# Kernel optimization log

Measured on AMD Instinct MI355X. Metric: run time of the kernel, lower is better.

Reference implementation:

```python
import jax, jax.numpy as jnp
import numpy as np

NQ, NKV, D = 32, 8, 64
HID = 2048
EPS = 1e-5
THETA = 1000000.0


def _rmsnorm(x, w):
    var = jnp.mean(x * x, axis=-1, keepdims=True)
    return x * jax.lax.rsqrt(var + EPS) * w


def setup_inputs() -> dict:
    key = jax.random.key(0)
    k1, k2, k3 = jax.random.split(key, 3)
    T = 2048
    positions = jnp.arange(T, dtype=jnp.int64) if jax.config.jax_enable_x64 else jnp.arange(T, dtype=jnp.int32)
    hidden_states = jax.random.normal(k1, (T, HID), dtype=jnp.float32)
    w_qkv = jax.random.normal(k2, (HID, (NQ + 2 * NKV) * D), dtype=jnp.float32) / np.sqrt(HID)
    w_out = jax.random.normal(k3, (NQ * D, HID), dtype=jnp.float32) / np.sqrt(NQ * D)
    q_ln_w = jnp.ones((D,), dtype=jnp.float32)
    k_ln_w = jnp.ones((D,), dtype=jnp.float32)
    return {"positions": positions, "hidden_states": hidden_states, "w_qkv": w_qkv,
            "w_out": w_out, "q_ln_w": q_ln_w, "k_ln_w": k_ln_w}


def reference(positions, hidden_states, w_qkv, w_out, q_ln_w, k_ln_w):
    T = hidden_states.shape[0]
    qkv = hidden_states @ w_qkv  # [T, (NQ+2*NKV)*D]
    q = qkv[:, : NQ * D].reshape(T, NQ, D)
    k = qkv[:, NQ * D : (NQ + NKV) * D].reshape(T, NKV, D)
    v = qkv[:, (NQ + NKV) * D :].reshape(T, NKV, D)
    # per-head RMSNorm on q and k
    q = _rmsnorm(q, q_ln_w)
    k = _rmsnorm(k, k_ln_w)
    # neox-style RoPE (rotate halves)
    inv_freq = 1.0 / (THETA ** (jnp.arange(0, D, 2, dtype=jnp.float32) / D))
    ang = positions.astype(jnp.float32)[:, None] * inv_freq  # [T, D/2]
    cos = jnp.cos(ang)[:, None, :]
    sin = jnp.sin(ang)[:, None, :]
    def rope(x):
        x1, x2 = x[..., : D // 2], x[..., D // 2 :]
        return jnp.concatenate([x1 * cos - x2 * sin, x2 * cos + x1 * sin], axis=-1)
    q = rope(q)
    k = rope(k)
    # grouped-query causal attention (one sequence, positions define order)
    G = NQ // NKV
    qg = q.reshape(T, NKV, G, D)
    scores = jnp.einsum('tkgd,skd->kgts', qg, k) * (D ** -0.5)  # [NKV,G,T,T]
    causal = jnp.arange(T)[:, None] >= jnp.arange(T)[None, :]
    scores = jnp.where(causal[None, None], scores, -1e30)
    probs = jax.nn.softmax(scores, axis=-1)
    attn = jnp.einsum('kgts,skd->tkgd', probs, v).reshape(T, NQ * D)
    return attn @ w_out
```

## Files before the change

kernel.cpp:

```cpp
#include <hip/hip_runtime.h>

typedef __bf16 bhalf;
typedef __bf16 bhalf8 __attribute__((ext_vector_type(8)));
typedef __bf16 bhalf4 __attribute__((ext_vector_type(4)));
typedef float f32x4 __attribute__((ext_vector_type(4)));

typedef __attribute__((address_space(1))) const void* gas_p;
typedef __attribute__((address_space(3))) void* las_p;

#define T_SEQ 2048
#define HIDN  2048
#define NQH   32
#define NKVH  8
#define DH    64
#define NQKV  3072

__global__ __launch_bounds__(256) void prep_k(const float* __restrict__ hidden,
                                              const float* __restrict__ w_qkv,
                                              const float* __restrict__ w_out,
                                              const int* __restrict__ pos,
                                              bhalf* __restrict__ hid_bf,
                                              bhalf* __restrict__ wqkvT,
                                              bhalf* __restrict__ woutT,
                                              float* __restrict__ rope) {
  __shared__ float tile[32][33];
  int bid = blockIdx.x;
  if (bid < 4096) {
    int i = (bid * 256 + threadIdx.x) * 4;
    float4 v = *(const float4*)(hidden + i);
    bhalf4 o;
    o[0] = (bhalf)v.x; o[1] = (bhalf)v.y; o[2] = (bhalf)v.z; o[3] = (bhalf)v.w;
    *(bhalf4*)(hid_bf + i) = o;
    return;
  }
  if (bid >= 14336) {
    int gid = (bid - 14336) * 256 + threadIdx.x;
    int t = gid >> 4, j = gid & 15;
    float p = (float)pos[t];
    float f0 = exp2f((float)j * -0.6228615177913804f);
    float a0 = p * f0, a1 = p * f0 * 0.001f;
    float4 cs = {cosf(a0), sinf(a0), cosf(a1), sinf(a1)};
    *(float4*)(rope + (size_t)gid * 4) = cs;
    return;
  }
  const float* in;
  bhalf* out;
  int R, C, bx, by;
  if (bid < 10240) {
    int b2 = bid - 4096;
    in = w_qkv; out = wqkvT; R = HIDN; C = NQKV;
    bx = (b2 % 96) * 32; by = (b2 / 96) * 32;
  } else {
    int b2 = bid - 10240;
    in = w_out; out = woutT; R = HIDN; C = HIDN;
    bx = (b2 % 64) * 32; by = (b2 / 64) * 32;
  }
  int tx = threadIdx.x & 31, ty = threadIdx.x >> 5;
#pragma unroll
  for (int p = 0; p < 4; ++p)
    tile[ty + 8 * p][tx] = in[(size_t)(by + ty + 8 * p) * C + bx + tx];
  __syncthreads();
#pragma unroll
  for (int p = 0; p < 4; ++p)
    out[(size_t)(bx + ty + 8 * p) * R + by + tx] = (bhalf)tile[tx][ty + 8 * p];
}

#define MFMA_BF16 __builtin_amdgcn_mfma_f32_16x16x32_bf16

#define GEMM_KS(ks)                                                            \
  {                                                                            \
    const int co_ = (((ks) * 4 + q4) ^ swz_) * 8;                              \
    bhalf8 af0 = *(const bhalf8*)&As[(wm_ +  0 + m16) * 64 + co_];             \
    bhalf8 af1 = *(const bhalf8*)&As[(wm_ + 16 + m16) * 64 + co_];             \
    bhalf8 af2 = *(const bhalf8*)&As[(wm_ + 32 + m16) * 64 + co_];             \
    bhalf8 af3 = *(const bhalf8*)&As[(wm_ + 48 + m16) * 64 + co_];             \
    bhalf8 bf0 = *(const bhalf8*)&Bs[(wn_ +  0 + m16) * 64 + co_];             \
    bhalf8 bf1 = *(const bhalf8*)&Bs[(wn_ + 16 + m16) * 64 + co_];             \
    bhalf8 bf2 = *(const bhalf8*)&Bs[(wn_ + 32 + m16) * 64 + co_];             \
    bhalf8 bf3 = *(const bhalf8*)&Bs[(wn_ + 48 + m16) * 64 + co_];             \
    acc[0][0] = MFMA_BF16(af0, bf0, acc[0][0], 0, 0, 0);                       \
    acc[0][1] = MFMA_BF16(af0, bf1, acc[0][1], 0, 0, 0);                       \
    acc[0][2] = MFMA_BF16(af0, bf2, acc[0][2], 0, 0, 0);                       \
    acc[0][3] = MFMA_BF16(af0, bf3, acc[0][3], 0, 0, 0);                       \
    acc[1][0] = MFMA_BF16(af1, bf0, acc[1][0], 0, 0, 0);                       \
    acc[1][1] = MFMA_BF16(af1, bf1, acc[1][1], 0, 0, 0);                       \
    acc[1][2] = MFMA_BF16(af1, bf2, acc[1][2], 0, 0, 0);                       \
    acc[1][3] = MFMA_BF16(af1, bf3, acc[1][3], 0, 0, 0);                       \
    acc[2][0] = MFMA_BF16(af2, bf0, acc[2][0], 0, 0, 0);                       \
    acc[2][1] = MFMA_BF16(af2, bf1, acc[2][1], 0, 0, 0);                       \
    acc[2][2] = MFMA_BF16(af2, bf2, acc[2][2], 0, 0, 0);                       \
    acc[2][3] = MFMA_BF16(af2, bf3, acc[2][3], 0, 0, 0);                       \
    acc[3][0] = MFMA_BF16(af3, bf0, acc[3][0], 0, 0, 0);                       \
    acc[3][1] = MFMA_BF16(af3, bf1, acc[3][1], 0, 0, 0);                       \
    acc[3][2] = MFMA_BF16(af3, bf2, acc[3][2], 0, 0, 0);                       \
    acc[3][3] = MFMA_BF16(af3, bf3, acc[3][3], 0, 0, 0);                       \
  }

#define GEMM_CORE_128(Aptr, Bptr, KK)                                          \
  {                                                                            \
    const int srow_ = tid >> 3;                                                \
    const int scol_ = ((tid & 7) ^ (srow_ & 7)) * 8;                           \
    const bhalf* asrc_ = (Aptr) + (size_t)(bm + srow_) * (KK) + scol_;         \
    const bhalf* bsrc_ = (Bptr) + (size_t)(bn + srow_) * (KK) + scol_;         \
    bhalf* adst_ = As + (wv * 8) * 64;                                         \
    bhalf* bdst_ = Bs + (wv * 8) * 64;                                         \
    const int swz_ = m16 & 7;                                                  \
    const int wm_ = (wv >> 1) * 64, wn_ = (wv & 1) * 64;                       \
    for (int k0 = 0; k0 < (KK); k0 += 64) {                                    \
      __syncthreads();            \
      _Pragma("unroll")                                                        \
      for (int c = 0; c < 4; ++c) {                                            \
        __builtin_amdgcn_global_load_lds(                                      \
            (gas_p)(asrc_ + (size_t)(c * 32) * (KK) + k0),                     \
            (las_p)(adst_ + c * 2048), 16, 0, 0);                              \
        __builtin_amdgcn_global_load_lds(                                      \
            (gas_p)(bsrc_ + (size_t)(c * 32) * (KK) + k0),                     \
            (las_p)(bdst_ + c * 2048), 16, 0, 0);                              \
      }                                                                        \
      __syncthreads();         \
      GEMM_KS(0)                                                               \
      GEMM_KS(1)                                                               \
    }                                                                          \
  }

__global__ __launch_bounds__(256, 1) void gemm1_fused_k(const bhalf* __restrict__ A,
                                                        const bhalf* __restrict__ Bt,
                                                        const float* __restrict__ rope,
                                                        const float* __restrict__ qw,
                                                        const float* __restrict__ kw,
                                                        bhalf* __restrict__ qo,
                                                        bhalf* __restrict__ ko,
                                                        bhalf* __restrict__ vt) {
  __shared__ __align__(16) bhalf As[8192];
  __shared__ __align__(16) bhalf Bs[8192];
  int tid = threadIdx.x, lane = tid & 63, wv = tid >> 6;
  int m16 = lane & 15, q4 = lane >> 4;
  int orig = blockIdx.x;
  int wgid = (orig & 7) * 48 + (orig >> 3);
  int bx = wgid % 24, by = wgid / 24;
  int bm = by * 128, bn = bx * 128;
  f32x4 zero4 = {0.f, 0.f, 0.f, 0.f};
  f32x4 acc[4][4];
#pragma unroll
  for (int mi = 0; mi < 4; ++mi)
#pragma unroll
    for (int ni = 0; ni < 4; ++ni) acc[mi][ni] = zero4;

  GEMM_CORE_128(A, Bt, HIDN)

  int r0 = bm + (wv >> 1) * 64;
  int hh = (bn >> 6) + (wv & 1);
  if (hh < 40) {
    float wd[4];
    const float* wptr = (hh < 32) ? qw : kw;
    float wscale = (hh < 32) ? 0.18033688011112042f : 1.0f;
#pragma unroll
    for (int ni = 0; ni < 4; ++ni) wd[ni] = wptr[ni * 16 + m16] * wscale;
#pragma unroll
    for (int mi = 0; mi < 4; ++mi)
#pragma unroll
      for (int r = 0; r < 4; ++r) {
        int trow = r0 + mi * 16 + q4 * 4 + r;
        float x0 = acc[mi][0][r], x1 = acc[mi][1][r], x2 = acc[mi][2][r], x3 = acc[mi][3][r];
        float ss = x0 * x0 + x1 * x1 + x2 * x2 + x3 * x3;
        ss += __shfl_xor(ss, 1);
        ss += __shfl_xor(ss, 2);
        ss += __shfl_xor(ss, 4);
        ss += __shfl_xor(ss, 8);
        float sc = rsqrtf(ss * (1.0f / 64.0f) + 1e-5f);
        float y0 = x0 * sc * wd[0], y1 = x1 * sc * wd[1];
        float y2 = x2 * sc * wd[2], y3 = x3 * sc * wd[3];
        float4 cs = *(const float4*)(rope + ((size_t)trow * 16 + m16) * 4);
        float o0 = y0 * cs.x - y2 * cs.y, o2 = y2 * cs.x + y0 * cs.y;
        float o1 = y1 * cs.z - y3 * cs.w, o3 = y3 * cs.z + y1 * cs.w;
        bhalf* dst = (hh < 32) ? (qo + (size_t)trow * 2048 + hh * 64 + m16)
                               : (ko + (size_t)trow * 512 + (hh - 32) * 64 + m16);
        dst[0] = (bhalf)o0; dst[16] = (bhalf)o1; dst[32] = (bhalf)o2; dst[48] = (bhalf)o3;
      }
  } else {
#pragma unroll
    for (int mi = 0; mi < 4; ++mi)
#pragma unroll
      for (int ni = 0; ni < 4; ++ni) {
        int trow0 = r0 + mi * 16 + q4 * 4;
        int d = (hh - 40) * 64 + ni * 16 + m16;
        bhalf4 pk;
        pk[0] = (bhalf)acc[mi][ni][0]; pk[1] = (bhalf)acc[mi][ni][1];
        pk[2] = (bhalf)acc[mi][ni][2]; pk[3] = (bhalf)acc[mi][ni][3];
        *(bhalf4*)(vt + (size_t)d * 2048 + trow0) = pk;
      }
  }
}

__global__ __launch_bounds__(256, 1) void gemm2_k(const bhalf* __restrict__ A,
                                                  const bhalf* __restrict__ Bt,
                                                  float* __restrict__ C) {
  __shared__ __align__(16) bhalf As[8192];
  __shared__ __align__(16) bhalf Bs[8192];
  int tid = threadIdx.x, lane = tid & 63, wv = tid >> 6;
  int m16 = lane & 15, q4 = lane >> 4;
  int orig = blockIdx.x;
  int wgid = (orig & 7) * 32 + (orig >> 3);
  int bx = wgid & 15, by = wgid >> 4;
  int bm = by * 128, bn = bx * 128;
  f32x4 zero4 = {0.f, 0.f, 0.f, 0.f};
  f32x4 acc[4][4];
#pragma unroll
  for (int mi = 0; mi < 4; ++mi)
#pragma unroll
    for (int ni = 0; ni < 4; ++ni) acc[mi][ni] = zero4;

  GEMM_CORE_128(A, Bt, HIDN)

  int r0 = bm + (wv >> 1) * 64;
  int c0 = bn + (wv & 1) * 64;
#pragma unroll
  for (int mi = 0; mi < 4; ++mi)
#pragma unroll
    for (int r = 0; r < 4; ++r) {
      size_t base = (size_t)(r0 + mi * 16 + q4 * 4 + r) * 2048 + c0 + m16;
      C[base] = acc[mi][0][r]; C[base + 16] = acc[mi][1][r];
      C[base + 32] = acc[mi][2][r]; C[base + 48] = acc[mi][3][r];
    }
}

__global__ __launch_bounds__(256) void attn_k(const bhalf* __restrict__ q,
                                              const bhalf* __restrict__ k,
                                              const bhalf* __restrict__ vt,
                                              bhalf* __restrict__ o) {
  __shared__ __align__(16) bhalf Kb[2][4096];
  __shared__ __align__(16) bhalf Vb[2][4096];
  __shared__ __align__(16) bhalf Pb[4][16][64];
  int tid = threadIdx.x, lane = tid & 63, w = tid >> 6;
  int h = blockIdx.x, kh = h >> 2;
  int qt = 31 - blockIdx.y;
  int qb = qt * 64;
  int m16 = lane & 15, q4 = lane >> 4;
  int wrow0 = qb + w * 16;

  const bhalf* qp = q + (size_t)(wrow0 + m16) * 2048 + h * 64;
  bhalf8 qf0 = *(const bhalf8*)(qp + q4 * 8);
  bhalf8 qf1 = *(const bhalf8*)(qp + 32 + q4 * 8);

  int srow = tid >> 3;
  int scol = ((tid & 7) ^ (srow & 7)) * 8;
  const bhalf* ksrc = k + (size_t)srow * 512 + kh * 64 + scol;
  const bhalf* vsrc = vt + (size_t)(kh * 64 + srow) * 2048 + scol;
  bhalf* kdst = &Kb[0][0] + w * 512;
  bhalf* vdst = &Vb[0][0] + w * 512;

  auto stage = [&](int c) {
    int buf = c & 1, s0 = c * 64;
#pragma unroll
    for (int j = 0; j < 2; ++j) {
      __builtin_amdgcn_global_load_lds((gas_p)(ksrc + (size_t)(s0 + j * 32) * 512),
                                       (las_p)(kdst + buf * 4096 + j * 2048), 16, 0, 0);
      __builtin_amdgcn_global_load_lds((gas_p)(vsrc + (size_t)(j * 32) * 2048 + s0),
                                       (las_p)(vdst + buf * 4096 + j * 2048), 16, 0, 0);
    }
  };

  f32x4 zero4 = {0.f, 0.f, 0.f, 0.f};
  f32x4 oac[4];
  float psum = 0.f;
#pragma unroll
  for (int ni = 0; ni < 4; ++ni) oac[ni] = zero4;
  int swz = m16 & 7;
  bhalf* prow = &Pb[w][m16][0];
  int woff = (q4 & 1) << 2;

  stage(0);
  for (int c = 0; c <= qt; ++c) {
    __syncthreads();
    if (c < qt) stage(c + 1);
    int buf = c & 1;
    if (c < qt) {
      bhalf8 kf[4][2];
#pragma unroll
      for (int st = 0; st < 4; ++st)
#pragma unroll
        for (int ks = 0; ks < 2; ++ks)
          kf[st][ks] = *(const bhalf8*)&Kb[buf][(st * 16 + m16) * 64 + (((ks * 4 + q4) ^ swz) * 8)];
      f32x4 sv[4];
      __builtin_amdgcn_s_setprio(1);
#pragma unroll
      for (int st = 0; st < 4; ++st) {
        f32x4 t0 = __builtin_amdgcn_mfma_f32_16x16x32_bf16(kf[st][0], qf0, zero4, 0, 0, 0);
        sv[st] = __builtin_amdgcn_mfma_f32_16x16x32_bf16(kf[st][1], qf1, t0, 0, 0, 0);
      }
      __builtin_amdgcn_s_setprio(0);
#pragma unroll
      for (int st = 0; st < 4; ++st) {
        bhalf4 pk;
#pragma unroll
        for (int r = 0; r < 4; ++r) {
          float pe = exp2f(sv[st][r]);
          psum += pe;
          pk[r] = (bhalf)pe;
        }
        *(bhalf4*)(prow + ((((2 * st + (q4 >> 1)) ^ swz) << 3) + woff)) = pk;
      }
      bhalf8 vf[4][2];
#pragma unroll
      for (int ni = 0; ni < 4; ++ni)
#pragma unroll
        for (int ks = 0; ks < 2; ++ks)
          vf[ni][ks] = *(const bhalf8*)&Vb[buf][(ni * 16 + m16) * 64 + (((ks * 4 + q4) ^ swz) * 8)];
      bhalf8 ap0 = *(const bhalf8*)(prow + ((q4 ^ swz) << 3));
      bhalf8 ap1 = *(const bhalf8*)(prow + (((4 + q4) ^ swz) << 3));
      __builtin_amdgcn_s_setprio(1);
#pragma unroll
      for (int ni = 0; ni < 4; ++ni) {
        oac[ni] = __builtin_amdgcn_mfma_f32_16x16x32_bf16(ap0, vf[ni][0], oac[ni], 0, 0, 0);
        oac[ni] = __builtin_amdgcn_mfma_f32_16x16x32_bf16(ap1, vf[ni][1], oac[ni], 0, 0, 0);
      }
      __builtin_amdgcn_s_setprio(0);
    } else {
      bhalf8 kf[4][2];
      f32x4 sv[4];
#pragma unroll
      for (int st = 0; st < 4; ++st)
        if (st <= w) {
#pragma unroll
          for (int ks = 0; ks < 2; ++ks)
            kf[st][ks] = *(const bhalf8*)&Kb[buf][(st * 16 + m16) * 64 + (((ks * 4 + q4) ^ swz) * 8)];
          f32x4 t0 = __builtin_amdgcn_mfma_f32_16x16x32_bf16(kf[st][0], qf0, zero4, 0, 0, 0);
          sv[st] = __builtin_amdgcn_mfma_f32_16x16x32_bf16(kf[st][1], qf1, t0, 0, 0, 0);
        }
      int stwr = (w >= 2) ? 3 : 1;
#pragma unroll
      for (int st = 0; st < 4; ++st) {
        if (st > stwr) continue;
        bhalf4 pk;
#pragma unroll
        for (int r = 0; r < 4; ++r) {
          float pe = 0.f;
          if (st < w) {
            pe = exp2f(sv[st][r]);
          } else if (st == w) {
            pe = (q4 * 4 + r <= m16) ? exp2f(sv[st][r]) : 0.f;
          }
          psum += pe;
          pk[r] = (bhalf)pe;
        }
        *(bhalf4*)(prow + ((((2 * st + (q4 >> 1)) ^ swz) << 3) + woff)) = pk;
      }
      int ksmax = (w >= 2) ? 1 : 0;
      bhalf8 vf[4][2];
#pragma unroll
      for (int ni = 0; ni < 4; ++ni)
#pragma unroll
        for (int ks = 0; ks < 2; ++ks)
          if (ks <= ksmax)
            vf[ni][ks] = *(const bhalf8*)&Vb[buf][(ni * 16 + m16) * 64 + (((ks * 4 + q4) ^ swz) * 8)];
      bhalf8 ap0 = *(const bhalf8*)(prow + ((q4 ^ swz) << 3));
#pragma unroll
      for (int ni = 0; ni < 4; ++ni)
        oac[ni] = __builtin_amdgcn_mfma_f32_16x16x32_bf16(ap0, vf[ni][0], oac[ni], 0, 0, 0);
      if (ksmax) {
        bhalf8 ap1 = *(const bhalf8*)(prow + (((4 + q4) ^ swz) << 3));
#pragma unroll
        for (int ni = 0; ni < 4; ++ni)
          oac[ni] = __builtin_amdgcn_mfma_f32_16x16x32_bf16(ap1, vf[ni][1], oac[ni], 0, 0, 0);
      }
    }
  }
  psum += __shfl_xor(psum, 16);
  psum += __shfl_xor(psum, 32);
  float inv = 1.0f / psum;
  float invr[4];
#pragma unroll
  for (int r = 0; r < 4; ++r) invr[r] = __shfl(inv, q4 * 4 + r);
#pragma unroll
  for (int ni = 0; ni < 4; ++ni)
#pragma unroll
    for (int r = 0; r < 4; ++r) {
      int trow = wrow0 + q4 * 4 + r;
      o[(size_t)trow * 2048 + h * 64 + ni * 16 + m16] = (bhalf)(oac[ni][r] * invr[r]);
    }
}

extern "C" void kernel_launch(void* const* d_in, const int* in_sizes, int n_in,
                              void* d_out, int out_size, void* d_ws, size_t ws_size,
                              hipStream_t stream) {
  const int* positions = (const int*)d_in[0];
  const float* hidden  = (const float*)d_in[1];
  const float* w_qkv   = (const float*)d_in[2];
  const float* w_out   = (const float*)d_in[3];
  const float* q_ln    = (const float*)d_in[4];
  const float* k_ln    = (const float*)d_in[5];
  float* out = (float*)d_out;

  char* wsp = (char*)d_ws;
  bhalf* hid_bf  = (bhalf*)(wsp);
  bhalf* wqkvT   = (bhalf*)(wsp + 8388608);
  bhalf* woutT   = (bhalf*)(wsp + 20971520);
  bhalf* q_bf    = (bhalf*)(wsp + 29360128);
  bhalf* k_bf    = (bhalf*)(wsp + 37748736);
  bhalf* vt_g    = (bhalf*)(wsp + 41943040);
  bhalf* attn_bf = (bhalf*)(wsp + 44040192);
  float* rope_t  = (float*)(wsp + 44040192);

  prep_k<<<14464, 256, 0, stream>>>(hidden, w_qkv, w_out, positions,
                                    hid_bf, wqkvT, woutT, rope_t);
  gemm1_fused_k<<<384, 256, 0, stream>>>(
      hid_bf, wqkvT, rope_t, q_ln, k_ln, q_bf, k_bf, vt_g);
  attn_k<<<dim3(NQH, 32), 256, 0, stream>>>(q_bf, k_bf, vt_g, attn_bf);
  gemm2_k<<<256, 256, 0, stream>>>(attn_bf, woutT, out);
}
```

Baseline: 223.1 us.

## Double-buffer GEMM LDS tiles and widen weight transpose tiles to 64x64

The shared GEMM core now uses two LDS buffers, so the next 64-wide K slice is fetched with global_load_lds while MFMAs run on the current one. This replaces the two barriers per iteration that serialized loads and math. Separately, the weight transpose/cast kernel moves from 32x32 to 64x64 tiles, with float4 loads and bf16x2 stores, cutting block count and raising access width. LDS per GEMM block doubles to 64KB, and the transposed tile store may see more bank conflicts.

After: 215.2 us. 3.5% less time.

```diff
diff --git a/kernel.cpp b/kernel.cpp
--- a/kernel.cpp
+++ b/kernel.cpp
@@ -3,6 +3,7 @@
 typedef __bf16 bhalf;
 typedef __bf16 bhalf8 __attribute__((ext_vector_type(8)));
 typedef __bf16 bhalf4 __attribute__((ext_vector_type(4)));
+typedef __bf16 bhalf2 __attribute__((ext_vector_type(2)));
 typedef float f32x4 __attribute__((ext_vector_type(4)));
 
 typedef __attribute__((address_space(1))) const void* gas_p;
@@ -23,18 +24,19 @@
                                               bhalf* __restrict__ wqkvT,
                                               bhalf* __restrict__ woutT,
                                               float* __restrict__ rope) {
-  __shared__ float tile[32][33];
+  __shared__ float tile[64][65];
   int bid = blockIdx.x;
+  int tx = threadIdx.x;
   if (bid < 4096) {
-    int i = (bid * 256 + threadIdx.x) * 4;
+    int i = (bid * 256 + tx) * 4;
     float4 v = *(const float4*)(hidden + i);
     bhalf4 o;
     o[0] = (bhalf)v.x; o[1] = (bhalf)v.y; o[2] = (bhalf)v.z; o[3] = (bhalf)v.w;
     *(bhalf4*)(hid_bf + i) = o;
     return;
   }
-  if (bid >= 14336) {
-    int gid = (bid - 14336) * 256 + threadIdx.x;
+  if (bid >= 6656) {
+    int gid = (bid - 6656) * 256 + tx;
     int t = gid >> 4, j = gid & 15;
     float p = (float)pos[t];
     float f0 = exp2f((float)j * -0.6228615177913804f);
@@ -46,38 +48,59 @@
   const float* in;
   bhalf* out;
   int R, C, bx, by;
-  if (bid < 10240) {
+  if (bid < 5632) {
     int b2 = bid - 4096;
     in = w_qkv; out = wqkvT; R = HIDN; C = NQKV;
-    bx = (b2 % 96) * 32; by = (b2 / 96) * 32;
+    bx = (b2 % 48) * 64; by = (b2 / 48) * 64;
   } else {
-    int b2 = bid - 10240;
+    int b2 = bid - 5632;
     in = w_out; out = woutT; R = HIDN; C = HIDN;
-    bx = (b2 % 64) * 32; by = (b2 / 64) * 32;
-  }
-  int tx = threadIdx.x & 31, ty = threadIdx.x >> 5;
-#pragma unroll
-  for (int p = 0; p < 4; ++p)
-    tile[ty + 8 * p][tx] = in[(size_t)(by + ty + 8 * p) * C + bx + tx];
+    bx = (b2 % 32) * 64; by = (b2 / 32) * 64;
+  }
+#pragma unroll
+  for (int p = 0; p < 4; ++p) {
+    int row = p * 16 + (tx >> 4);
+    int col = (tx & 15) * 4;
+    float4 v = *(const float4*)(in + (size_t)(by + row) * C + bx + col);
+    tile[row][col] = v.x; tile[row][col + 1] = v.y;
+    tile[row][col + 2] = v.z; tile[row][col + 3] = v.w;
+  }
   __syncthreads();
 #pragma unroll
-  for (int p = 0; p < 4; ++p)
-    out[(size_t)(bx + ty + 8 * p) * R + by + tx] = (bhalf)tile[tx][ty + 8 * p];
+  for (int p = 0; p < 8; ++p) {
+    int c = p * 8 + (tx >> 5);
+    int rp = tx & 31;
+    bhalf2 o2;
+    o2[0] = (bhalf)tile[2 * rp][c];
+    o2[1] = (bhalf)tile[2 * rp + 1][c];
+    *(bhalf2*)(out + (size_t)(bx + c) * R + by + 2 * rp) = o2;
+  }
 }
 
 #define MFMA_BF16 __builtin_amdgcn_mfma_f32_16x16x32_bf16
 
-#define GEMM_KS(ks)                                                            \
+#define GEMM_STAGE(Aps, Bps, k0)                                               \
+  _Pragma("unroll")                                                            \
+  for (int c = 0; c < 4; ++c) {                                                \
+    __builtin_amdgcn_global_load_lds(                                          \
+        (gas_p)(asrc_ + (size_t)(c * 32) * 2048 + (k0)),                       \
+        (las_p)(Aps + woff_ + c * 2048), 16, 0, 0);                            \
+    __builtin_amdgcn_global_load_lds(                                          \
+        (gas_p)(bsrc_ + (size_t)(c * 32) * 2048 + (k0)),                       \
+        (las_p)(Bps + woff_ + c * 2048), 16, 0, 0);                            \
+  }
+
+#define GEMM_KS(Aps, Bps, ks)                                                  \
   {                                                                            \
     const int co_ = (((ks) * 4 + q4) ^ swz_) * 8;                              \
-    bhalf8 af0 = *(const bhalf8*)&As[(wm_ +  0 + m16) * 64 + co_];             \
-    bhalf8 af1 = *(const bhalf8*)&As[(wm_ + 16 + m16) * 64 + co_];             \
-    bhalf8 af2 = *(const bhalf8*)&As[(wm_ + 32 + m16) * 64 + co_];             \
-    bhalf8 af3 = *(const bhalf8*)&As[(wm_ + 48 + m16) * 64 + co_];             \
-    bhalf8 bf0 = *(const bhalf8*)&Bs[(wn_ +  0 + m16) * 64 + co_];             \
-    bhalf8 bf1 = *(const bhalf8*)&Bs[(wn_ + 16 + m16) * 64 + co_];             \
-    bhalf8 bf2 = *(const bhalf8*)&Bs[(wn_ + 32 + m16) * 64 + co_];             \
-    bhalf8 bf3 = *(const bhalf8*)&Bs[(wn_ + 48 + m16) * 64 + co_];             \
+    bhalf8 af0 = *(const bhalf8*)&Aps[(wm_ +  0 + m16) * 64 + co_];            \
+    bhalf8 af1 = *(const bhalf8*)&Aps[(wm_ + 16 + m16) * 64 + co_];            \
+    bhalf8 af2 = *(const bhalf8*)&Aps[(wm_ + 32 + m16) * 64 + co_];            \
+    bhalf8 af3 = *(const bhalf8*)&Aps[(wm_ + 48 + m16) * 64 + co_];            \
+    bhalf8 bf0 = *(const bhalf8*)&Bps[(wn_ +  0 + m16) * 64 + co_];            \
+    bhalf8 bf1 = *(const bhalf8*)&Bps[(wn_ + 16 + m16) * 64 + co_];            \
+    bhalf8 bf2 = *(const bhalf8*)&Bps[(wn_ + 32 + m16) * 64 + co_];            \
+    bhalf8 bf3 = *(const bhalf8*)&Bps[(wn_ + 48 + m16) * 64 + co_];            \
     acc[0][0] = MFMA_BF16(af0, bf0, acc[0][0], 0, 0, 0);                       \
     acc[0][1] = MFMA_BF16(af0, bf1, acc[0][1], 0, 0, 0);                       \
     acc[0][2] = MFMA_BF16(af0, bf2, acc[0][2], 0, 0, 0);                       \
@@ -96,30 +119,25 @@
     acc[3][3] = MFMA_BF16(af3, bf3, acc[3][3], 0, 0, 0);                       \
   }
 
-#define GEMM_CORE_128(Aptr, Bptr, KK)                                          \
+#define GEMM_CORE_128DB(Aptr, Bptr)                                            \
   {                                                                            \
     const int srow_ = tid >> 3;                                                \
     const int scol_ = ((tid & 7) ^ (srow_ & 7)) * 8;                           \
-    const bhalf* asrc_ = (Aptr) + (size_t)(bm + srow_) * (KK) + scol_;         \
-    const bhalf* bsrc_ = (Bptr) + (size_t)(bn + srow_) * (KK) + scol_;         \
-    bhalf* adst_ = As + (wv * 8) * 64;                                         \
-    bhalf* bdst_ = Bs + (wv * 8) * 64;                                         \
+    const bhalf* asrc_ = (Aptr) + (size_t)(bm + srow_) * 2048 + scol_;         \
+    const bhalf* bsrc_ = (Bptr) + (size_t)(bn + srow_) * 2048 + scol_;         \
+    const int woff_ = wv * 512;                                                \
     const int swz_ = m16 & 7;                                                  \
     const int wm_ = (wv >> 1) * 64, wn_ = (wv & 1) * 64;                       \
-    for (int k0 = 0; k0 < (KK); k0 += 64) {                                    \
-      __syncthreads();            \
-      _Pragma("unroll")                                                        \
-      for (int c = 0; c < 4; ++c) {                                            \
-        __builtin_amdgcn_global_load_lds(                                      \
-            (gas_p)(asrc_ + (size_t)(c * 32) * (KK) + k0),                     \
-            (las_p)(adst_ + c * 2048), 16, 0, 0);                              \
-        __builtin_amdgcn_global_load_lds(                                      \
-            (gas_p)(bsrc_ + (size_t)(c * 32) * (KK) + k0),                     \
-            (las_p)(bdst_ + c * 2048), 16, 0, 0);                              \
-      }                                                                        \
-      __syncthreads();         \
-      GEMM_KS(0)                                                               \
-      GEMM_KS(1)                                                               \
+    GEMM_STAGE(As0, Bs0, 0)                                                    \
+    for (int k0 = 0; k0 < 2048; k0 += 128) {                                   \
+      __syncthreads();                 \
+      GEMM_STAGE(As1, Bs1, k0 + 64)            \
+      GEMM_KS(As0, Bs0, 0)                                                     \
+      GEMM_KS(As0, Bs0, 1)                                                     \
+      __syncthreads();                 \
+      if (k0 + 128 < 2048) GEMM_STAGE(As0, Bs0, k0 + 128)                      \
+      GEMM_KS(As1, Bs1, 0)                                                     \
+      GEMM_KS(As1, Bs1, 1)                                                     \
     }                                                                          \
   }
 
@@ -131,8 +149,7 @@
                                                         bhalf* __restrict__ qo,
                                                         bhalf* __restrict__ ko,
                                                         bhalf* __restrict__ vt) {
-  __shared__ __align__(16) bhalf As[8192];
-  __shared__ __align__(16) bhalf Bs[8192];
+  __shared__ __align__(16) bhalf As0[8192], Bs0[8192], As1[8192], Bs1[8192];
   int tid = threadIdx.x, lane = tid & 63, wv = tid >> 6;
   int m16 = lane & 15, q4 = lane >> 4;
   int orig = blockIdx.x;
@@ -146,7 +163,7 @@
 #pragma unroll
     for (int ni = 0; ni < 4; ++ni) acc[mi][ni] = zero4;
 
-  GEMM_CORE_128(A, Bt, HIDN)
+  GEMM_CORE_128DB(A, Bt)
 
   int r0 = bm + (wv >> 1) * 64;
   int hh = (bn >> 6) + (wv & 1);
@@ -195,8 +212,7 @@
 __global__ __launch_bounds__(256, 1) void gemm2_k(const bhalf* __restrict__ A,
                                                   const bhalf* __restrict__ Bt,
                                                   float* __restrict__ C) {
-  __shared__ __align__(16) bhalf As[8192];
-  __shared__ __align__(16) bhalf Bs[8192];
+  __shared__ __align__(16) bhalf As0[8192], Bs0[8192], As1[8192], Bs1[8192];
   int tid = threadIdx.x, lane = tid & 63, wv = tid >> 6;
   int m16 = lane & 15, q4 = lane >> 4;
   int orig = blockIdx.x;
@@ -210,7 +226,7 @@
 #pragma unroll
     for (int ni = 0; ni < 4; ++ni) acc[mi][ni] = zero4;
 
-  GEMM_CORE_128(A, Bt, HIDN)
+  GEMM_CORE_128DB(A, Bt)
 
   int r0 = bm + (wv >> 1) * 64;
   int c0 = bn + (wv & 1) * 64;
@@ -401,8 +417,8 @@
   bhalf* attn_bf = (bhalf*)(wsp + 44040192);
   float* rope_t  = (float*)(wsp + 44040192);
 
-  prep_k<<<14464, 256, 0, stream>>>(hidden, w_qkv, w_out, positions,
-                                    hid_bf, wqkvT, woutT, rope_t);
+  prep_k<<<6784, 256, 0, stream>>>(hidden, w_qkv, w_out, positions,
+                                   hid_bf, wqkvT, woutT, rope_t);
   gemm1_fused_k<<<384, 256, 0, stream>>>(
       hid_bf, wqkvT, rope_t, q_ln, k_ln, q_bf, k_bf, vt_g);
   attn_k<<<dim3(NQH, 32), 256, 0, stream>>>(q_bf, k_bf, vt_g, attn_bf);
```
